# Kernel optimization log

Measured on AMD Instinct MI355X. Metric: run time of the kernel, lower is better.

## Reference

```python
import jax, jax.numpy as jnp
import numpy as np

EMBED_DIM = 1024
NUM_HEADS = 8
HEAD_DIM = EMBED_DIM // NUM_HEADS
SCALING = HEAD_DIM ** -0.5
SEQ_LEN = 2048
BATCH = 4


def setup_inputs() -> dict:
    key = jax.random.key(0)
    ks = jax.random.split(key, 12)
    s = 0.02
    d = EMBED_DIM
    return {
        "q": jax.random.normal(ks[0], (SEQ_LEN, BATCH, d), jnp.float32),
        "k": jax.random.normal(ks[1], (SEQ_LEN, BATCH, d), jnp.float32),
        "v": jax.random.normal(ks[2], (SEQ_LEN, BATCH, d), jnp.float32),
        # Linear weights stored as (in, out): y = x @ W + b
        "Wq": jax.random.normal(ks[3], (d, d), jnp.float32) * s,
        "bq": jnp.zeros((d,), jnp.float32),
        "Wk": jax.random.normal(ks[4], (d, d), jnp.float32) * s,
        "bk": jnp.zeros((d,), jnp.float32),
        "Wv": jax.random.normal(ks[5], (d, d), jnp.float32) * s,
        "bv": jnp.zeros((d,), jnp.float32),
        "Wo": jax.random.normal(ks[6], (d, d), jnp.float32) * s,
        "bo": jnp.zeros((d,), jnp.float32),
    }


def _to_head(x):
    # 'l n (h e) -> n h l e'
    l, n, _ = x.shape
    return x.reshape(l, n, NUM_HEADS, HEAD_DIM).transpose(1, 2, 0, 3)


def reference(q, k, v, Wq, bq, Wk, bk, Wv, bv, Wo, bo):
    l = q.shape[0]  # src_len
    m = k.shape[0]  # tgt_len
    qp = (q @ Wq + bq) * SCALING          # (l, n, d)
    kp = k @ Wk + bk                       # (m, n, d)
    vp = v @ Wv + bv                       # (m, n, d) -- V shared across heads
    qh = _to_head(qp)                      # (n, h, l, e)
    kh = _to_head(kp)                      # (n, h, m, e)
    scores = jnp.einsum('nhle,nhme->nhlm', qh, kh)  # (n, h, l, m)
    mask = jnp.triu(jnp.ones((l, m), bool), k=1)    # True above diagonal
    scores = jnp.where(mask[None, None], -jnp.inf, scores)
    w = jax.nn.softmax(scores, axis=-1)    # (n, h, l, m)
    w_mean = w.mean(axis=1)                # head-averaged weights (n, l, m)
    attn = jnp.einsum('nlm,mne->lne', w_mean, vp)   # (l, n, d)
    out = attn @ Wo + bo                   # (l, n, d)
    return out, w_mean
```

## Files before the change

kernel.cpp:

```cpp
#include <hip/hip_runtime.h>


#define L_SEQ 2048
#define NBATCH 4
#define DMODEL 1024
#define NHEAD 8
#define SCALING 0.08838834764831845f
#define NQ (2048L * 4 * 1024)

typedef _Float16 f16x8 __attribute__((ext_vector_type(8)));
typedef float f32x4 __attribute__((ext_vector_type(4)));

#define GLOBAL_AS __attribute__((address_space(1)))
#define LDS_AS __attribute__((address_space(3)))

__device__ __forceinline__ unsigned short f2h_bits(float x) {
  _Float16 h = (_Float16)x;
  return __builtin_bit_cast(unsigned short, h);
}

__device__ __forceinline__ void gl_lds16(const void* g, void* l) {
  __builtin_amdgcn_global_load_lds((GLOBAL_AS void*)g, (LDS_AS void*)l, 16, 0, 0);
}

__global__ __launch_bounds__(256) void prep(
    const float* __restrict__ Wq, const float* __restrict__ Wk,
    const float* __restrict__ Wo,
    _Float16* __restrict__ WqT, _Float16* __restrict__ WkT,
    _Float16* __restrict__ WoT,
    const float* __restrict__ bv, float* __restrict__ bvo,
    float4* __restrict__ Zsum4)
{
  const int z = (int)blockIdx.z;
  const int tid = threadIdx.y * 32 + threadIdx.x;
  if (z == 3) {
    if (blockIdx.y == 0 && blockIdx.x < 4) {
      int j = blockIdx.x * 256 + tid;
      float acc = 0.f;
      for (int i = 0; i < DMODEL; ++i) acc += bv[i] * Wo[(long)i * DMODEL + j];
      bvo[j] = acc;
    } else if (blockIdx.y == 1 || blockIdx.y == 2) {
      long idx = ((long)(blockIdx.y - 1) * 32 + blockIdx.x) * 256 + tid;
      if (idx < (long)NBATCH * NHEAD * L_SEQ / 4)
        Zsum4[idx] = (float4){0.f, 0.f, 0.f, 0.f};
    }
    return;
  }
  __shared__ _Float16 tile[32][33];
  const float* in = z == 0 ? Wq : (z == 1 ? Wk : Wo);
  _Float16* outp = z == 0 ? WqT : (z == 1 ? WkT : WoT);
  int r0 = blockIdx.y * 32, c0 = blockIdx.x * 32;
  for (int i = threadIdx.y; i < 32; i += 8)
    tile[i][threadIdx.x] = (_Float16)in[(long)(r0 + i) * 1024 + c0 + threadIdx.x];
  __syncthreads();
  for (int i = threadIdx.y; i < 32; i += 8)
    outp[(long)(c0 + i) * 1024 + r0 + threadIdx.x] = tile[threadIdx.x][i];
}

__global__ __launch_bounds__(256) void cvt3(
    const float* __restrict__ q, const float* __restrict__ k,
    const float* __restrict__ v, _Float16* __restrict__ xh)
{
  long i = ((long)blockIdx.x * 256 + threadIdx.x) * 8;
  if (i >= 3 * NQ) return;
  int which = (int)(i / NQ);
  const float* src = which == 0 ? q : (which == 1 ? k : v);
  long off = i - (long)which * NQ;
  float4 a = *(const float4*)(src + off);
  float4 b = *(const float4*)(src + off + 4);
  f16x8 h;
  h[0] = (_Float16)a.x; h[1] = (_Float16)a.y; h[2] = (_Float16)a.z; h[3] = (_Float16)a.w;
  h[4] = (_Float16)b.x; h[5] = (_Float16)b.y; h[6] = (_Float16)b.z; h[7] = (_Float16)b.w;
  *(f16x8*)(xh + i) = h;
}

template <bool AF16, bool BF16>
__global__ __launch_bounds__(256) void gemm16(
    const void* __restrict__ Ap, long lda, long a_bs,
    const void* __restrict__ Bp, long ldb, long b_bs,
    float* __restrict__ C, long ldc, long c_bs,
    _Float16* __restrict__ Ch, long ldch, long ch_bs,
    const float* __restrict__ bias, int bias_row, float alpha, int K,
    int causal, int cmode)
{
  __shared__ __align__(16) _Float16 As[128][64];
  __shared__ __align__(16) _Float16 Bs[128][64];
  const int tid = threadIdx.x;
  const int lane = tid & 63, wv = tid >> 6;
  const int g = lane >> 4, cc = lane & 15;
  const int wm = wv >> 1, wn = wv & 1;
  const long m0 = (long)blockIdx.y * 128;
  const long n0 = (long)blockIdx.x * 128;

  const float* Af = nullptr; const _Float16* Ah = nullptr;
  const float* Bf = nullptr; const _Float16* Bh = nullptr;
  if constexpr (AF16) Ah = (const _Float16*)Ap + (long)blockIdx.z * a_bs;
  else                Af = (const float*)Ap + (long)blockIdx.z * a_bs;
  if constexpr (BF16) Bh = (const _Float16*)Bp + (long)blockIdx.z * b_bs;
  else                Bf = (const float*)Bp + (long)blockIdx.z * b_bs;

  int Keff = K;
  if (causal) { int lim = (int)m0 + 128; if (lim < K) Keff = lim; }
  const int NT = Keff >> 6;

  f32x4 acc[4][4] = {};
  char* AsB = (char*)&As[0][0];
  char* BsB = (char*)&Bs[0][0];

  for (int kt = 0; kt < NT; ++kt) {
    const long k0 = (long)kt << 6;
    __syncthreads();
    if constexpr (AF16) {
#pragma unroll
      for (int i = 0; i < 4; ++i) {
        int r = 32 * wv + 8 * i + (lane >> 3);
        int gc = (lane & 7) ^ (r & 7);
        gl_lds16(Ah + (m0 + r) * lda + k0 + gc * 8, &As[32 * wv + 8 * i][0]);
      }
    } else {
#pragma unroll
      for (int p = 0; p < 8; ++p) {
        int r = p * 16 + (tid >> 4);
        float4 vv = *(const float4*)(Af + (m0 + r) * lda + k0 + (tid & 15) * 4);
        ushort4 hh;
        hh.x = f2h_bits(vv.x); hh.y = f2h_bits(vv.y);
        hh.z = f2h_bits(vv.z); hh.w = f2h_bits(vv.w);
        *(ushort4*)(AsB + r * 128 + (((tid & 15) * 8) ^ ((r & 7) << 4))) = hh;
      }
    }
    if constexpr (BF16) {
#pragma unroll
      for (int i = 0; i < 4; ++i) {
        int r = 32 * wv + 8 * i + (lane >> 3);
        int gc = (lane & 7) ^ (r & 7);
        gl_lds16(Bh + (n0 + r) * ldb + k0 + gc * 8, &Bs[32 * wv + 8 * i][0]);
      }
    } else {
#pragma unroll
      for (int p = 0; p < 8; ++p) {
        int r = p * 16 + (tid >> 4);
        float4 vv = *(const float4*)(Bf + (n0 + r) * ldb + k0 + (tid & 15) * 4);
        ushort4 hh;
        hh.x = f2h_bits(vv.x); hh.y = f2h_bits(vv.y);
        hh.z = f2h_bits(vv.z); hh.w = f2h_bits(vv.w);
        *(ushort4*)(BsB + r * 128 + (((tid & 15) * 8) ^ ((r & 7) << 4))) = hh;
      }
    }
    __syncthreads();
#pragma unroll
    for (int s = 0; s < 2; ++s) {
      f16x8 af[4], bfr[4];
#pragma unroll
      for (int mi = 0; mi < 4; ++mi) {
        int r = wm * 64 + mi * 16 + cc;
        af[mi] = *(const f16x8*)(AsB + r * 128 + ((s * 64 + 16 * g) ^ ((r & 7) << 4)));
      }
#pragma unroll
      for (int ni = 0; ni < 4; ++ni) {
        int r = wn * 64 + ni * 16 + cc;
        bfr[ni] = *(const f16x8*)(BsB + r * 128 + ((s * 64 + 16 * g) ^ ((r & 7) << 4)));
      }
#pragma unroll
      for (int mi = 0; mi < 4; ++mi)
#pragma unroll
        for (int ni = 0; ni < 4; ++ni)
          acc[mi][ni] = __builtin_amdgcn_mfma_f32_16x16x32_f16(af[mi], bfr[ni], acc[mi][ni], 0, 0, 0);
    }
  }

  float* Cp = C ? C + (long)blockIdx.z * c_bs : nullptr;
  _Float16* Chp = Ch ? Ch + (long)blockIdx.z * ch_bs : nullptr;
#pragma unroll
  for (int ni = 0; ni < 4; ++ni) {
    long col = n0 + wn * 64 + ni * 16 + cc;
    float bcol = (bias && !bias_row) ? bias[col] : 0.0f;
#pragma unroll
    for (int mi = 0; mi < 4; ++mi) {
      long row0 = m0 + wm * 64 + mi * 16 + 4 * g;
#pragma unroll
      for (int rg = 0; rg < 4; ++rg) {
        long row = row0 + rg;
        float b = (bias && bias_row) ? bias[row] : bcol;
        float vv = (acc[mi][ni][rg] + b) * alpha;
        if (Cp) Cp[row * ldc + col] = vv;
        if (Chp) {
          if (cmode == 1) {
            long idx = (((row & 3) * NHEAD + (col >> 7)) * (long)L_SEQ + (row >> 2)) * 128 +
                       (col & 127);
            Chp[idx] = (_Float16)vv;
          } else {
            Chp[row * ldch + col] = (_Float16)vv;
          }
        }
      }
    }
  }
}

__global__ __launch_bounds__(256) void projqk(
    const _Float16* __restrict__ xh, const _Float16* __restrict__ WqT,
    const _Float16* __restrict__ WkT, const float* __restrict__ bq,
    const float* __restrict__ bk, _Float16* __restrict__ qph,
    _Float16* __restrict__ kph)
{
  __shared__ __align__(16) _Float16 As[64][64];
  __shared__ __align__(16) _Float16 Bs[128][64];
  const int tid = threadIdx.x, lane = tid & 63, wv = tid >> 6;
  const int g = lane >> 4, cc = lane & 15;
  const int wm = wv >> 1, wn = wv & 1;
  const int sel = (int)blockIdx.y;
  const _Float16* A = xh + (long)sel * NQ;
  const _Float16* B = sel ? WkT : WqT;
  const float* bias = sel ? bk : bq;
  const float alpha = sel ? 1.0f : SCALING;
  _Float16* dst = sel ? kph : qph;
  const int bid = (int)blockIdx.x;
  const int j = bid >> 3;
  const int mt = (bid & 7) * 16 + (j & 15);
  const int nt = j >> 4;
  const long m0 = (long)mt * 64;
  const long n0 = (long)nt * 128;

  f32x4 acc[2][4] = {};
  char* AsB = (char*)&As[0][0];
  char* BsB = (char*)&Bs[0][0];

  for (int kt = 0; kt < 16; ++kt) {
    const long k0 = (long)kt << 6;
    __syncthreads();
#pragma unroll
    for (int i = 0; i < 2; ++i) {
      int r = 16 * wv + 8 * i + (lane >> 3);
      int gc = (lane & 7) ^ (r & 7);
      gl_lds16(A + (m0 + r) * 1024 + k0 + gc * 8, &As[16 * wv + 8 * i][0]);
    }
#pragma unroll
    for (int i = 0; i < 4; ++i) {
      int r = 32 * wv + 8 * i + (lane >> 3);
      int gc = (lane & 7) ^ (r & 7);
      gl_lds16(B + (n0 + r) * 1024 + k0 + gc * 8, &Bs[32 * wv + 8 * i][0]);
    }
    __syncthreads();
#pragma unroll
    for (int s = 0; s < 2; ++s) {
      f16x8 af[2], bfr[4];
#pragma unroll
      for (int mi = 0; mi < 2; ++mi) {
        int r = wm * 32 + mi * 16 + cc;
        af[mi] = *(const f16x8*)(AsB + r * 128 + ((s * 64 + 16 * g) ^ ((r & 7) << 4)));
      }
#pragma unroll
      for (int ni = 0; ni < 4; ++ni) {
        int r = wn * 64 + ni * 16 + cc;
        bfr[ni] = *(const f16x8*)(BsB + r * 128 + ((s * 64 + 16 * g) ^ ((r & 7) << 4)));
      }
#pragma unroll
      for (int mi = 0; mi < 2; ++mi)
#pragma unroll
        for (int ni = 0; ni < 4; ++ni)
          acc[mi][ni] = __builtin_amdgcn_mfma_f32_16x16x32_f16(af[mi], bfr[ni], acc[mi][ni], 0, 0, 0);
    }
  }

#pragma unroll
  for (int ni = 0; ni < 4; ++ni) {
    long col = n0 + wn * 64 + ni * 16 + cc;
    float bcol = bias[col];
#pragma unroll
    for (int mi = 0; mi < 2; ++mi) {
      long row0 = m0 + wm * 32 + mi * 16 + 4 * g;
#pragma unroll
      for (int rg = 0; rg < 4; ++rg) {
        long row = row0 + rg;
        float vv = (acc[mi][ni][rg] + bcol) * alpha;
        long idx = (((row & 3) * NHEAD + (col >> 7)) * (long)L_SEQ + (row >> 2)) * 128 +
                   (col & 127);
        dst[idx] = (_Float16)vv;
      }
    }
  }
}

__global__ __launch_bounds__(256) void proj64(
    const _Float16* __restrict__ Ap, long lda, long a_bs,
    const _Float16* __restrict__ Bp, long ldb, long b_bs,
    _Float16* __restrict__ Ch, long ldch, long ch_bs,
    const float* __restrict__ bias, int bias_row, float alpha, int K,
    int cmode, int ntiles)
{
  __shared__ __align__(16) _Float16 As[64][64];
  __shared__ __align__(16) _Float16 Bs[128][64];
  const int tid = threadIdx.x, lane = tid & 63, wv = tid >> 6;
  const int g = lane >> 4, cc = lane & 15;
  const int wm = wv >> 1, wn = wv & 1;
  const int fi = (int)blockIdx.x;
  const int by = fi / ntiles, nc = fi % ntiles;
  const long m0 = (long)by * 64;
  const long n0 = (long)nc * 128;
  const _Float16* A = Ap + (long)blockIdx.z * a_bs;
  const _Float16* B = Bp + (long)blockIdx.z * b_bs;
  const int NT = K >> 6;

  f32x4 acc[2][4] = {};
  char* AsB = (char*)&As[0][0];
  char* BsB = (char*)&Bs[0][0];

  for (int kt = 0; kt < NT; ++kt) {
    const long k0 = (long)kt << 6;
    __syncthreads();
#pragma unroll
    for (int i = 0; i < 2; ++i) {
      int r = 16 * wv + 8 * i + (lane >> 3);
      int gc = (lane & 7) ^ (r & 7);
      gl_lds16(A + (m0 + r) * lda + k0 + gc * 8, &As[16 * wv + 8 * i][0]);
    }
#pragma unroll
    for (int i = 0; i < 4; ++i) {
      int r = 32 * wv + 8 * i + (lane >> 3);
      int gc = (lane & 7) ^ (r & 7);
      gl_lds16(B + (n0 + r) * ldb + k0 + gc * 8, &Bs[32 * wv + 8 * i][0]);
    }
    __syncthreads();
#pragma unroll
    for (int s = 0; s < 2; ++s) {
      f16x8 af[2], bfr[4];
#pragma unroll
      for (int mi = 0; mi < 2; ++mi) {
        int r = wm * 32 + mi * 16 + cc;
        af[mi] = *(const f16x8*)(AsB + r * 128 + ((s * 64 + 16 * g) ^ ((r & 7) << 4)));
      }
#pragma unroll
      for (int ni = 0; ni < 4; ++ni) {
        int r = wn * 64 + ni * 16 + cc;
        bfr[ni] = *(const f16x8*)(BsB + r * 128 + ((s * 64 + 16 * g) ^ ((r & 7) << 4)));
      }
#pragma unroll
      for (int mi = 0; mi < 2; ++mi)
#pragma unroll
        for (int ni = 0; ni < 4; ++ni)
          acc[mi][ni] = __builtin_amdgcn_mfma_f32_16x16x32_f16(af[mi], bfr[ni], acc[mi][ni], 0, 0, 0);
    }
  }

  _Float16* Chp = Ch + (long)blockIdx.z * ch_bs;
#pragma unroll
  for (int ni = 0; ni < 4; ++ni) {
    long col = n0 + wn * 64 + ni * 16 + cc;
    float bcol = bias_row ? 0.0f : bias[col];
#pragma unroll
    for (int mi = 0; mi < 2; ++mi) {
      long row0 = m0 + wm * 32 + mi * 16 + 4 * g;
#pragma unroll
      for (int rg = 0; rg < 4; ++rg) {
        long row = row0 + rg;
        float b = bias_row ? bias[row] : bcol;
        float vv = (acc[mi][ni][rg] + b) * alpha;
        if (cmode == 1) {
          long idx = (((row & 3) * NHEAD + (col >> 7)) * (long)L_SEQ + (row >> 2)) * 128 +
                     (col & 127);
          Chp[idx] = (_Float16)vv;
        } else {
          Chp[row * ldch + col] = (_Float16)vv;
        }
      }
    }
  }
}

__global__ __launch_bounds__(256) void out_gemm16(
    const _Float16* __restrict__ wm16, const _Float16* __restrict__ voT,
    const float* __restrict__ bo, float* __restrict__ out)
{
  __shared__ __align__(16) _Float16 As[64][128];
  __shared__ __align__(16) _Float16 Bs[128][128];
  const int tid = threadIdx.x, lane = tid & 63, wv = tid >> 6;
  const int g = lane >> 4, cc = lane & 15;
  const int wm = wv >> 1, wn = wv & 1;
  const int bid = (int)blockIdx.x;
  const int j = bid >> 3;
  const int p = (j >> 3) * 8 + (bid & 7);
  const int by = 31 - (p >> 2);
  const int nb = p & 3;
  const int nc = j & 7;
  const long m0 = (long)by * 64;
  const long n0 = (long)nc * 128;
  const _Float16* A = wm16 + (long)nb * L_SEQ * L_SEQ;
  const _Float16* B = voT + (long)nb * 2048L * 1024;
  const int NT = (by + 2) >> 1;
  const int srow = lane >> 4, scl = lane & 15;

  f32x4 acc[2][4] = {};
  char* AsB = (char*)&As[0][0];
  char* BsB = (char*)&Bs[0][0];

  for (int kt = 0; kt < NT; ++kt) {
    const long k0 = (long)kt << 7;
    __syncthreads();
#pragma unroll
    for (int i = 0; i < 4; ++i) {
      int r = 16 * wv + 4 * i + srow;
      int gc = scl ^ (r & 7);
      gl_lds16(A + (m0 + r) * 2048 + k0 + gc * 8, &As[16 * wv + 4 * i][0]);
    }
#pragma unroll
    for (int i = 0; i < 8; ++i) {
      int r = 32 * wv + 4 * i + srow;
      int gc = scl ^ (r & 7);
      gl_lds16(B + (n0 + r) * 2048 + k0 + gc * 8, &Bs[32 * wv + 4 * i][0]);
    }
    __syncthreads();
#pragma unroll
    for (int s = 0; s < 4; ++s) {
      f16x8 af[2], bfr[4];
#pragma unroll
      for (int mi = 0; mi < 2; ++mi) {
        int r = wm * 32 + mi * 16 + cc;
        af[mi] = *(const f16x8*)(AsB + r * 256 + (((4 * s + g) ^ (r & 7)) << 4));
      }
#pragma unroll
      for (int ni = 0; ni < 4; ++ni) {
        int r = wn * 64 + ni * 16 + cc;
        bfr[ni] = *(const f16x8*)(BsB + r * 256 + (((4 * s + g) ^ (r & 7)) << 4));
      }
#pragma unroll
      for (int mi = 0; mi < 2; ++mi)
#pragma unroll
        for (int ni = 0; ni < 4; ++ni)
          acc[mi][ni] = __builtin_amdgcn_mfma_f32_16x16x32_f16(af[mi], bfr[ni], acc[mi][ni], 0, 0, 0);
    }
  }

#pragma unroll
  for (int ni = 0; ni < 4; ++ni) {
    long col = n0 + wn * 64 + ni * 16 + cc;
    float b = bo[col];
#pragma unroll
    for (int mi = 0; mi < 2; ++mi) {
      long l0 = m0 + wm * 32 + mi * 16 + 4 * g;
#pragma unroll
      for (int rg = 0; rg < 4; ++rg)
        out[(l0 + rg) * 4096 + nb * 1024 + col] = acc[mi][ni][rg] + b;
    }
  }
}

__global__ __launch_bounds__(256) void s1_kernel(
    const _Float16* __restrict__ qph, const _Float16* __restrict__ kph,
    float* __restrict__ Zsum)
{
  __shared__ __align__(16) _Float16 Qs[64][128];
  __shared__ __align__(16) _Float16 Ks[64][128];
  const int tid = threadIdx.x, lane = tid & 63, w = tid >> 6;
  const int g = lane >> 4, cc = lane & 15;
  const int h = blockIdx.y, nb = blockIdx.z;
  int fi = 79 - (int)blockIdx.x;
  int by, seg;
  if (fi < 8)       { by = fi;                  seg = 0; }
  else if (fi < 24) { int t = fi - 8;  by = 8  + (t >> 1); seg = t & 1; }
  else if (fi < 48) { int t = fi - 24; by = 16 + t / 3;    seg = t % 3; }
  else              { int t = fi - 48; by = 24 + (t >> 2); seg = t & 3; }
  const int lb = by * 64;
  const int c0 = seg * 8;
  const int cEnd = min(c0 + 8, by + 1);
  const int srow = lane >> 4, scl = lane & 15;
  const long hb = ((long)(nb * NHEAD + h)) * L_SEQ * 128;
  char* QsB = (char*)&Qs[0][0];
  char* KsB = (char*)&Ks[0][0];

#pragma unroll
  for (int i = 0; i < 4; ++i) {
    int r = 16 * w + 4 * i + srow;
    int gc = scl ^ (r & 7);
    gl_lds16(&qph[hb + (long)(lb + r) * 128 + gc * 8], &Qs[16 * w + 4 * i][0]);
  }
  auto stageK = [&](int ch) {
#pragma unroll
    for (int i = 0; i < 4; ++i) {
      int r = 16 * w + 4 * i + srow;
      int gc = scl ^ (r & 7);
      gl_lds16(&kph[hb + (long)(ch * 64 + r) * 128 + gc * 8], &Ks[16 * w + 4 * i][0]);
    }
  };
  stageK(c0);
  __syncthreads();

  f16x8 qf[4];
  {
    int r = 16 * w + cc;
#pragma unroll
    for (int s = 0; s < 4; ++s)
      qf[s] = *(const f16x8*)(QsB + r * 256 + ((64 * s + 16 * g) ^ ((r & 7) << 4)));
  }

  f32x4 zacc = {0.f, 0.f, 0.f, 0.f};
  const int l0 = lb + 16 * w + 4 * g;
  for (int ch = c0; ch < cEnd; ++ch) {
#pragma unroll
    for (int t = 0; t < 4; ++t) {
      int kr = 16 * t + cc;
      f32x4 acc = {0.f, 0.f, 0.f, 0.f};
#pragma unroll
      for (int s = 0; s < 4; ++s) {
        f16x8 kf = *(const f16x8*)(KsB + kr * 256 + ((64 * s + 16 * g) ^ ((kr & 7) << 4)));
        acc = __builtin_amdgcn_mfma_f32_16x16x32_f16(qf[s], kf, acc, 0, 0, 0);
      }
      int m = ch * 64 + 16 * t + cc;
#pragma unroll
      for (int rg = 0; rg < 4; ++rg) {
        float e = __expf(acc[rg]);
        zacc[rg] += (m <= l0 + rg) ? e : 0.f;
      }
    }
    if (ch + 1 < cEnd) {
      __syncthreads();
      stageK(ch + 1);
      __syncthreads();
    }
  }
#pragma unroll
  for (int rg = 0; rg < 4; ++rg) {
    float vv = zacc[rg];
    vv += __shfl_xor(vv, 1, 16);
    vv += __shfl_xor(vv, 2, 16);
    vv += __shfl_xor(vv, 4, 16);
    vv += __shfl_xor(vv, 8, 16);
    if (cc == 0)
      atomicAdd(&Zsum[((long)nb * NHEAD + h) * L_SEQ + l0 + rg], vv);
  }
}

__global__ __launch_bounds__(256) void zero_fill(float* __restrict__ wmean)
{
  int t = (int)blockIdx.x, nb = (int)blockIdx.y;
  int by = 0, rem = t;
  while (rem >= 15 - by) { rem -= 15 - by; ++by; }
  const int mc = by + 1 + rem;
  const int tr = threadIdx.x >> 1, th = threadIdx.x & 1;
  float4 z4 = {0.f, 0.f, 0.f, 0.f};
  float* p = wmean + (long)nb * L_SEQ * L_SEQ + (long)(by * 128 + tr) * L_SEQ +
             mc * 128 + th * 64;
#pragma unroll
  for (int j = 0; j < 16; ++j) ((float4*)p)[j] = z4;
}

__global__ __launch_bounds__(256) void s2_kernel(
    const _Float16* __restrict__ qph, const _Float16* __restrict__ kph,
    const float* __restrict__ Zsum, float* __restrict__ wmean,
    _Float16* __restrict__ wm16)
{
  __shared__ __align__(16) _Float16 Qs[64][128];
  __shared__ __align__(16) _Float16 Ks[128][128];
  __shared__ float zl[NHEAD][64];
  const int tid = threadIdx.x, lane = tid & 63, w = tid >> 6;
  const int g = lane >> 4, cc = lane & 15;
  const int nb = blockIdx.y;
  int b = (int)blockIdx.x;
  int bx = (b & 7) * 34 + (b >> 3);
  int rem = 271 - bx;
  int by = 0;
  while (rem >= (by >> 1) + 1) { rem -= (by >> 1) + 1; ++by; }
  const int mc = rem;
  const int lb = by * 64, mb = mc * 128;
  const bool diag = (mb + 127 > lb);
  const int srow = lane >> 4, scl = lane & 15;
  char* QsB = (char*)&Qs[0][0];
  char* KsB = (char*)&Ks[0][0];

  for (int i = tid; i < NHEAD * 64; i += 256)
    zl[i >> 6][i & 63] =
        1.0f / (8.0f * Zsum[((long)nb * NHEAD + (i >> 6)) * L_SEQ + lb + (i & 63)]);

  auto stage = [&](int h) {
    const long qb = ((long)(nb * NHEAD + h) * L_SEQ + lb) * 128;
    const long kb = ((long)(nb * NHEAD + h) * L_SEQ + mb) * 128;
#pragma unroll
    for (int i = 0; i < 4; ++i) {
      int r = 16 * w + 4 * i + srow;
      int gc = scl ^ (r & 7);
      gl_lds16(&qph[qb + (long)r * 128 + gc * 8], &Qs[16 * w + 4 * i][0]);
    }
#pragma unroll
    for (int i = 0; i < 8; ++i) {
      int r = 32 * w + 4 * i + srow;
      int gc = scl ^ (r & 7);
      gl_lds16(&kph[kb + (long)r * 128 + gc * 8], &Ks[32 * w + 4 * i][0]);
    }
  };
  stage(0);
  __syncthreads();

  f32x4 wacc[8] = {};
  const int l0 = lb + 16 * w + 4 * g;
  for (int h = 0; h < NHEAD; ++h) {
    f16x8 qf[4];
    int qr = 16 * w + cc;
#pragma unroll
    for (int s = 0; s < 4; ++s)
      qf[s] = *(const f16x8*)(QsB + qr * 256 + ((64 * s + 16 * g) ^ ((qr & 7) << 4)));
    f32x4 zv = *(const f32x4*)&zl[h][16 * w + 4 * g];
#pragma unroll
    for (int t = 0; t < 8; ++t) {
      int kr = 16 * t + cc;
      f32x4 acc = {0.f, 0.f, 0.f, 0.f};
#pragma unroll
      for (int s = 0; s < 4; ++s) {
        f16x8 kf = *(const f16x8*)(KsB + kr * 256 + ((64 * s + 16 * g) ^ ((kr & 7) << 4)));
        acc = __builtin_amdgcn_mfma_f32_16x16x32_f16(qf[s], kf, acc, 0, 0, 0);
      }
      int m = mb + 16 * t + cc;
#pragma unroll
      for (int rg = 0; rg < 4; ++rg) {
        float e = __expf(acc[rg]) * zv[rg];
        wacc[t][rg] += (!diag || m <= l0 + rg) ? e : 0.f;
      }
    }
    if (h + 1 < NHEAD) {
      __syncthreads();
      stage(h + 1);
      __syncthreads();
    }
  }
  float* wout = wmean + (long)nb * L_SEQ * L_SEQ;
  _Float16* w16 = wm16 + (long)nb * L_SEQ * L_SEQ;
#pragma unroll
  for (int t = 0; t < 8; ++t) {
    int m = mb + 16 * t + cc;
#pragma unroll
    for (int rg = 0; rg < 4; ++rg) {
      long idx = (long)(l0 + rg) * L_SEQ + m;
      wout[idx] = wacc[t][rg];
      w16[idx] = (_Float16)wacc[t][rg];
    }
  }
}

extern "C" void kernel_launch(void* const* d_in, const int* in_sizes, int n_in,
                              void* d_out, int out_size, void* d_ws, size_t ws_size,
                              hipStream_t stream)
{
  const float* q  = (const float*)d_in[0];
  const float* k  = (const float*)d_in[1];
  const float* v  = (const float*)d_in[2];
  const float* Wq = (const float*)d_in[3];
  const float* bq = (const float*)d_in[4];
  const float* Wk = (const float*)d_in[5];
  const float* bk = (const float*)d_in[6];
  const float* Wv = (const float*)d_in[7];
  const float* bv = (const float*)d_in[8];
  const float* Wo = (const float*)d_in[9];
  const float* bo = (const float*)d_in[10];

  float* out = (float*)d_out;
  float* wmean = out + (long)L_SEQ * NBATCH * DMODEL;

  if (ws_size < (140UL << 20)) return;

  char* ws = (char*)d_ws;
  _Float16* xh   = (_Float16*)(ws);
  _Float16* qph  = (_Float16*)(ws + (48L << 20));
  _Float16* kph  = (_Float16*)(ws + (64L << 20));
  _Float16* voT  = (_Float16*)(ws + (80L << 20));
  _Float16* wm16 = (_Float16*)(ws + (96L << 20));
  _Float16* WqT  = (_Float16*)(ws + (130L << 20));
  _Float16* WkT  = (_Float16*)(ws + (132L << 20));
  _Float16* WoT  = (_Float16*)(ws + (134L << 20));
  _Float16* WvoT = (_Float16*)(ws + (136L << 20));
  float*    bvo  = (float*)   (ws + (138L << 20));
  float*    Zsum = (float*)   (ws + (138L << 20) + (1L << 16));

  prep<<<dim3(32, 32, 4), dim3(32, 8, 1), 0, stream>>>(
      Wq, Wk, Wo, WqT, WkT, WoT, bv, bvo, (float4*)Zsum);
  gemm16<true, false><<<dim3(8, 8, 1), 256, 0, stream>>>(
      WoT, 1024, 0, Wv, 1024, 0,
      (float*)nullptr, 0, 0, WvoT, 1024, 0,
      (const float*)nullptr, 0, 1.0f, 1024, 0, 0);
  cvt3<<<dim3(12288, 1, 1), 256, 0, stream>>>(q, k, v, xh);
  projqk<<<dim3(1024, 2, 1), 256, 0, stream>>>(xh, WqT, WkT, bq, bk, qph, kph);
  proj64<<<dim3(256, 1, 4), 256, 0, stream>>>(
      WvoT, 1024, 0, xh + 2 * NQ, 4096, 1024, voT, 2048, 2048L * 1024,
      bvo, 1, 1.0f, 1024, 0, 16);
  s1_kernel<<<dim3(80, NHEAD, NBATCH), 256, 0, stream>>>(qph, kph, Zsum);
  zero_fill<<<dim3(120, 4, 1), 256, 0, stream>>>(wmean);
  s2_kernel<<<dim3(272, NBATCH, 1), 256, 0, stream>>>(qph, kph, Zsum, wmean, wm16);
  out_gemm16<<<dim3(1024, 1, 1), 256, 0, stream>>>(wm16, voT, bo, out);
}
```

Before: 308.6 us.

## Fold wmean zero-fill into prep kernel and remap s2 tiles per XCD

The separate zero_fill launch for the masked upper-triangle blocks of wmean is removed and its work is done by an extra z-slice of the prep kernel, saving one kernel launch. The s2_kernel block-to-tile mapping is also rewritten so each XCD (blockIdx.x & 7) gets a paired set of column chunks (mc and 15-mc), balancing diagonal and full tiles across XCDs and possibly improving L2 locality of K tiles. The prep grid grows by 1024 blocks, most of which exit immediately.

Result: faster. 296.6 us (-3.9%).

```diff
diff --git a/kernel.cpp b/kernel.cpp
--- a/kernel.cpp
+++ b/kernel.cpp
@@ -29,10 +29,25 @@
     _Float16* __restrict__ WqT, _Float16* __restrict__ WkT,
     _Float16* __restrict__ WoT,
     const float* __restrict__ bv, float* __restrict__ bvo,
-    float4* __restrict__ Zsum4)
+    float4* __restrict__ Zsum4, float* __restrict__ wmean)
 {
   const int z = (int)blockIdx.z;
   const int tid = threadIdx.y * 32 + threadIdx.x;
+  if (z == 4) {
+    int i = blockIdx.y * 32 + blockIdx.x;
+    if (i >= 480) return;
+    int t = i % 120, nb = i / 120;
+    int by = 0, rem = t;
+    while (rem >= 15 - by) { rem -= 15 - by; ++by; }
+    const int mc = by + 1 + rem;
+    const int tr = tid >> 1, th = tid & 1;
+    float4 z4 = {0.f, 0.f, 0.f, 0.f};
+    float* p = wmean + (long)nb * L_SEQ * L_SEQ + (long)(by * 128 + tr) * L_SEQ +
+               mc * 128 + th * 64;
+#pragma unroll
+    for (int jj = 0; jj < 16; ++jj) ((float4*)p)[jj] = z4;
+    return;
+  }
   if (z == 3) {
     if (blockIdx.y == 0 && blockIdx.x < 4) {
       int j = blockIdx.x * 256 + tid;
@@ -529,20 +544,6 @@
   }
 }
 
-__global__ __launch_bounds__(256) void zero_fill(float* __restrict__ wmean)
-{
-  int t = (int)blockIdx.x, nb = (int)blockIdx.y;
-  int by = 0, rem = t;
-  while (rem >= 15 - by) { rem -= 15 - by; ++by; }
-  const int mc = by + 1 + rem;
-  const int tr = threadIdx.x >> 1, th = threadIdx.x & 1;
-  float4 z4 = {0.f, 0.f, 0.f, 0.f};
-  float* p = wmean + (long)nb * L_SEQ * L_SEQ + (long)(by * 128 + tr) * L_SEQ +
-             mc * 128 + th * 64;
-#pragma unroll
-  for (int j = 0; j < 16; ++j) ((float4*)p)[j] = z4;
-}
-
 __global__ __launch_bounds__(256) void s2_kernel(
     const _Float16* __restrict__ qph, const _Float16* __restrict__ kph,
     const float* __restrict__ Zsum, float* __restrict__ wmean,
@@ -554,12 +555,12 @@
   const int tid = threadIdx.x, lane = tid & 63, w = tid >> 6;
   const int g = lane >> 4, cc = lane & 15;
   const int nb = blockIdx.y;
-  int b = (int)blockIdx.x;
-  int bx = (b & 7) * 34 + (b >> 3);
-  int rem = 271 - bx;
-  int by = 0;
-  while (rem >= (by >> 1) + 1) { rem -= (by >> 1) + 1; ++by; }
-  const int mc = rem;
+  const int x = (int)blockIdx.x;
+  const int xcd = x & 7, idx = x >> 3;
+  const int cnt0 = 32 - 2 * xcd;
+  int mc, by;
+  if (idx < cnt0) { mc = xcd;      by = 31 - idx; }
+  else            { mc = 15 - xcd; by = 31 - (idx - cnt0); }
   const int lb = by * 64, mb = mc * 128;
   const bool diag = (mb + 127 > lb);
   const int srow = lane >> 4, scl = lane & 15;
@@ -627,9 +628,9 @@
     int m = mb + 16 * t + cc;
 #pragma unroll
     for (int rg = 0; rg < 4; ++rg) {
-      long idx = (long)(l0 + rg) * L_SEQ + m;
-      wout[idx] = wacc[t][rg];
-      w16[idx] = (_Float16)wacc[t][rg];
+      long idx2 = (long)(l0 + rg) * L_SEQ + m;
+      wout[idx2] = wacc[t][rg];
+      w16[idx2] = (_Float16)wacc[t][rg];
     }
   }
 }
@@ -668,8 +669,8 @@
   float*    bvo  = (float*)   (ws + (138L << 20));
   float*    Zsum = (float*)   (ws + (138L << 20) + (1L << 16));
 
-  prep<<<dim3(32, 32, 4), dim3(32, 8, 1), 0, stream>>>(
-      Wq, Wk, Wo, WqT, WkT, WoT, bv, bvo, (float4*)Zsum);
+  prep<<<dim3(32, 32, 5), dim3(32, 8, 1), 0, stream>>>(
+      Wq, Wk, Wo, WqT, WkT, WoT, bv, bvo, (float4*)Zsum, wmean);
   gemm16<true, false><<<dim3(8, 8, 1), 256, 0, stream>>>(
       WoT, 1024, 0, Wv, 1024, 0,
       (float*)nullptr, 0, 0, WvoT, 1024, 0,
@@ -680,7 +681,6 @@
       WvoT, 1024, 0, xh + 2 * NQ, 4096, 1024, voT, 2048, 2048L * 1024,
       bvo, 1, 1.0f, 1024, 0, 16);
   s1_kernel<<<dim3(80, NHEAD, NBATCH), 256, 0, stream>>>(qph, kph, Zsum);
-  zero_fill<<<dim3(120, 4, 1), 256, 0, stream>>>(wmean);
   s2_kernel<<<dim3(272, NBATCH, 1), 256, 0, stream>>>(qph, kph, Zsum, wmean, wm16);
   out_gemm16<<<dim3(1024, 1, 1), 256, 0, stream>>>(wm16, voT, bo, out);
 }
```
